# Kernel tuning notes

Hardware: AMD Instinct MI355X
Metric: run time of the kernel (lower is better)

The kernel has to match this reference:

```python
import jax, jax.numpy as jnp
import numpy as np

N = 100000
E = 1600000
D = 64  # in = hidden = out channels


def setup_inputs() -> dict:
    key = jax.random.key(0)
    ks = jax.random.split(key, 6)
    x = jax.random.normal(ks[0], (N, D), dtype=jnp.float32)
    edge_index = jax.random.randint(ks[1], (2, E), 0, N, dtype=jnp.int64)
    # bias-free linear weights, torch Linear layout [out, in]
    s = 1.0 / np.sqrt(D)
    W0 = jax.random.uniform(ks[2], (D, D), jnp.float32, -s, s)
    W1 = jax.random.uniform(ks[3], (D, D), jnp.float32, -s, s)
    Wm = jax.random.uniform(ks[4], (D, D), jnp.float32, -s, s)
    eps0 = jnp.zeros((), jnp.float32)  # train_eps=True, init 0.0
    eps1 = jnp.zeros((), jnp.float32)
    return {"x": x, "edge_index": edge_index, "W0": W0, "eps0": eps0,
            "W1": W1, "eps1": eps1, "Wm": Wm}


def reference(x, edge_index, W0, eps0, W1, eps1, Wm):
    n = x.shape[0]
    src, dst = edge_index[0], edge_index[1]

    def gin_conv(h, W, eps):
        # sparse adjacency sum-aggregation: out[i] = sum_{j->i} h[j]
        agg = jax.ops.segment_sum(h[src], dst, num_segments=n)
        # eps-scaled self-loop + bias-free linear
        return (agg + (1.0 + eps) * h) @ W.T

    h1 = jax.nn.relu(gin_conv(x, W0, eps0))   # xs[0], [N, D]
    h2 = jax.nn.relu(gin_conv(h1, W1, eps1))  # xs[1], [N, D]
    return (h1 @ Wm.T + h2) / 2.0
```

## Files before the change

### kernel.cpp

```cpp
#include <hip/hip_runtime.h>
#include <hip/hip_fp16.h>


__global__ __launch_bounds__(256) void zero_int_kernel(int* __restrict__ p, int n)
{
    int i = blockIdx.x * blockDim.x + threadIdx.x;
    int stride = gridDim.x * blockDim.x;
    for (; i < n; i += stride) p[i] = 0;
}

__global__ __launch_bounds__(256) void hist_rank_kernel(
    const int* __restrict__ dst, int* __restrict__ deg,
    int* __restrict__ rank, int E)
{
    int base = (blockIdx.x * blockDim.x + threadIdx.x) * 16;
    if (base + 15 < E) {
        int4 a = *(const int4*)&dst[base];
        int4 b = *(const int4*)&dst[base + 4];
        int4 c = *(const int4*)&dst[base + 8];
        int4 d = *(const int4*)&dst[base + 12];
        int r0 = atomicAdd(&deg[a.x], 1);
        int r1 = atomicAdd(&deg[a.y], 1);
        int r2 = atomicAdd(&deg[a.z], 1);
        int r3 = atomicAdd(&deg[a.w], 1);
        int r4 = atomicAdd(&deg[b.x], 1);
        int r5 = atomicAdd(&deg[b.y], 1);
        int r6 = atomicAdd(&deg[b.z], 1);
        int r7 = atomicAdd(&deg[b.w], 1);
        int r8 = atomicAdd(&deg[c.x], 1);
        int r9 = atomicAdd(&deg[c.y], 1);
        int rA = atomicAdd(&deg[c.z], 1);
        int rB = atomicAdd(&deg[c.w], 1);
        int rC = atomicAdd(&deg[d.x], 1);
        int rD = atomicAdd(&deg[d.y], 1);
        int rE = atomicAdd(&deg[d.z], 1);
        int rF = atomicAdd(&deg[d.w], 1);
        *(int4*)&rank[base]      = make_int4(r0, r1, r2, r3);
        *(int4*)&rank[base + 4]  = make_int4(r4, r5, r6, r7);
        *(int4*)&rank[base + 8]  = make_int4(r8, r9, rA, rB);
        *(int4*)&rank[base + 12] = make_int4(rC, rD, rE, rF);
    } else {
        for (int e = base; e < E; ++e) rank[e] = atomicAdd(&deg[dst[e]], 1);
    }
}

__global__ __launch_bounds__(256) void hist_kernel(
    const int* __restrict__ dst, int* __restrict__ deg, int E)
{
    int e4 = (blockIdx.x * blockDim.x + threadIdx.x) * 4;
    if (e4 + 3 < E) {
        int4 d = *(const int4*)&dst[e4];
        atomicAdd(&deg[d.x], 1);
        atomicAdd(&deg[d.y], 1);
        atomicAdd(&deg[d.z], 1);
        atomicAdd(&deg[d.w], 1);
    } else {
        for (int e = e4; e < E; ++e) atomicAdd(&deg[dst[e]], 1);
    }
}

__global__ __launch_bounds__(256) void scanA_kernel(
    const int* __restrict__ deg, int* __restrict__ off,
    int* __restrict__ bsum, int n)
{
    __shared__ int tmp[256];
    int t = threadIdx.x;
    int base = blockIdx.x * 1024 + t * 4;
    int v0 = 0, v1 = 0, v2 = 0, v3 = 0;
    if (base + 3 < n) {
        int4 q = *(const int4*)&deg[base];
        v0 = q.x; v1 = q.y; v2 = q.z; v3 = q.w;
    } else {
        if (base + 0 < n) v0 = deg[base + 0];
        if (base + 1 < n) v1 = deg[base + 1];
        if (base + 2 < n) v2 = deg[base + 2];
    }
    int tot = v0 + v1 + v2 + v3;
    tmp[t] = tot;
    __syncthreads();
    for (int d = 1; d < 256; d <<= 1) {
        int x = (t >= d) ? tmp[t - d] : 0;
        __syncthreads();
        tmp[t] += x;
        __syncthreads();
    }
    int incl = tmp[t];
    int p = incl - tot;
    if (base + 0 < n) off[base + 0] = p;
    if (base + 1 < n) off[base + 1] = p + v0;
    if (base + 2 < n) off[base + 2] = p + v0 + v1;
    if (base + 3 < n) off[base + 3] = p + v0 + v1 + v2;
    if (t == 255) bsum[blockIdx.x] = incl;
}

__global__ __launch_bounds__(256) void scanB_kernel(int* __restrict__ bsum, int nb)
{
    __shared__ int tmp[256];
    int t = threadIdx.x;
    int v = (t < nb) ? bsum[t] : 0;
    tmp[t] = v;
    __syncthreads();
    for (int d = 1; d < 256; d <<= 1) {
        int x = (t >= d) ? tmp[t - d] : 0;
        __syncthreads();
        tmp[t] += x;
        __syncthreads();
    }
    if (t < nb) bsum[t] = tmp[t] - v;
}

__global__ __launch_bounds__(256) void scanC_kernel(
    int* __restrict__ off, int* __restrict__ cursor,
    const int* __restrict__ bsum, int n, int E)
{
    int t = threadIdx.x;
    int add = bsum[blockIdx.x];
    int base = blockIdx.x * 1024 + t * 4;
#pragma unroll
    for (int q = 0; q < 4; ++q) {
        int idx = base + q;
        if (idx < n) {
            int v = off[idx] + add;
            off[idx] = v;
            if (cursor) cursor[idx] = v;
        }
    }
    if (blockIdx.x == 0 && t == 0) off[n] = E;
}

__global__ __launch_bounds__(256) void fill_rank_kernel(
    const int* __restrict__ src, const int* __restrict__ dst,
    const int* __restrict__ rank, const int* __restrict__ off,
    int* __restrict__ bucket, int E)
{
    int base = (blockIdx.x * blockDim.x + threadIdx.x) * 8;
    if (base + 7 < E) {
        int4 d0 = *(const int4*)&dst[base];
        int4 d1 = *(const int4*)&dst[base + 4];
        int4 r0 = *(const int4*)&rank[base];
        int4 r1 = *(const int4*)&rank[base + 4];
        int4 s0 = *(const int4*)&src[base];
        int4 s1 = *(const int4*)&src[base + 4];
        bucket[off[d0.x] + r0.x] = s0.x;
        bucket[off[d0.y] + r0.y] = s0.y;
        bucket[off[d0.z] + r0.z] = s0.z;
        bucket[off[d0.w] + r0.w] = s0.w;
        bucket[off[d1.x] + r1.x] = s1.x;
        bucket[off[d1.y] + r1.y] = s1.y;
        bucket[off[d1.z] + r1.z] = s1.z;
        bucket[off[d1.w] + r1.w] = s1.w;
    } else {
        for (int e = base; e < E; ++e) bucket[off[dst[e]] + rank[e]] = src[e];
    }
}

__global__ __launch_bounds__(256) void fill_kernel(
    const int* __restrict__ src, const int* __restrict__ dst,
    int* __restrict__ cursor, int* __restrict__ bucket, int E)
{
    int e = blockIdx.x * blockDim.x + threadIdx.x;
    if (e < E) {
        int d = dst[e];
        int p = atomicAdd(&cursor[d], 1);
        bucket[p] = src[e];
    }
}

__global__ __launch_bounds__(256) void f32_to_f16_kernel(
    const float* __restrict__ in, __half* __restrict__ out, int total4)
{
    int i = blockIdx.x * blockDim.x + threadIdx.x;
    int stride = gridDim.x * blockDim.x;
    const float4* in4 = (const float4*)in;
    uint2* out4 = (uint2*)out;
    for (; i < total4; i += stride) {
        float4 v = in4[i];
        __half2 a = __floats2half2_rn(v.x, v.y);
        __half2 b = __floats2half2_rn(v.z, v.w);
        uint2 u;
        u.x = __builtin_bit_cast(unsigned int, a);
        u.y = __builtin_bit_cast(unsigned int, b);
        out4[i] = u;
    }
}

#define WPB 8

__device__ __forceinline__ float dot4(float4 a, float4 b)
{
    return a.x * b.x + a.y * b.y + a.z * b.z + a.w * b.w;
}

__device__ __forceinline__ __half2 bc_h2(unsigned int u)
{
    return __builtin_bit_cast(__half2, u);
}

__global__ __launch_bounds__(512) void fused_gin_h_kernel(
    const __half* __restrict__ hh, const int* __restrict__ off,
    const int* __restrict__ bucket, const float* __restrict__ W,
    const float* __restrict__ eps, __half* __restrict__ outh, int n)
{
    __shared__ float Ws[64][68];
    __shared__ float P[WPB][4][64];
    __shared__ float rowbuf[WPB][64];
    int tid = threadIdx.x;
    for (int idx = tid; idx < 4096; idx += 512) Ws[idx >> 6][idx & 63] = W[idx];
    __syncthreads();
    float s = 1.0f + eps[0];
    int lane = tid & 63;
    int w = tid >> 6;
    int l16 = lane & 15;
    int g = lane >> 4;
    int wavesTotal = gridDim.x * WPB;
    for (int i = blockIdx.x * WPB + w; i < n; i += wavesTotal) {
        int2 be = *(const int2*)&off[i];
        int beg = __builtin_amdgcn_readfirstlane(be.x);
        int end = __builtin_amdgcn_readfirstlane(be.y);
        __half2 ha = bc_h2(0u), hb = bc_h2(0u);
        float4 acc4 = make_float4(0.f, 0.f, 0.f, 0.f);
        int j = beg;
        for (; j + 8 <= end; j += 8) {
            int sa = bucket[j + g];
            int sb = bucket[j + 4 + g];
            uint2 va = *(const uint2*)&hh[(size_t)sa * 64 + l16 * 4];
            uint2 vb = *(const uint2*)&hh[(size_t)sb * 64 + l16 * 4];
            ha = __hadd2(__hadd2(ha, bc_h2(va.x)), bc_h2(vb.x));
            hb = __hadd2(__hadd2(hb, bc_h2(va.y)), bc_h2(vb.y));
        }
        if (j + 4 <= end) {
            int sa = bucket[j + g];
            uint2 va = *(const uint2*)&hh[(size_t)sa * 64 + l16 * 4];
            ha = __hadd2(ha, bc_h2(va.x));
            hb = __hadd2(hb, bc_h2(va.y));
            j += 4;
        }
        if (j < end) {
            int jj = j + g;
            int sc = bucket[(jj < end) ? jj : (end - 1)];
            float m = (jj < end) ? 1.0f : 0.0f;
            uint2 vc = *(const uint2*)&hh[(size_t)sc * 64 + l16 * 4];
            float2 c01 = __half22float2(bc_h2(vc.x));
            float2 c23 = __half22float2(bc_h2(vc.y));
            acc4.x = fmaf(c01.x, m, acc4.x);
            acc4.y = fmaf(c01.y, m, acc4.y);
            acc4.z = fmaf(c23.x, m, acc4.z);
            acc4.w = fmaf(c23.y, m, acc4.w);
        }
        float2 f01 = __half22float2(ha);
        float2 f23 = __half22float2(hb);
        acc4.x += f01.x; acc4.y += f01.y; acc4.z += f23.x; acc4.w += f23.y;
        if (g == 0) {
            uint2 sv = *(const uint2*)&hh[(size_t)i * 64 + l16 * 4];
            float2 s01 = __half22float2(bc_h2(sv.x));
            float2 s23 = __half22float2(bc_h2(sv.y));
            acc4.x = fmaf(s01.x, s, acc4.x);
            acc4.y = fmaf(s01.y, s, acc4.y);
            acc4.z = fmaf(s23.x, s, acc4.z);
            acc4.w = fmaf(s23.y, s, acc4.w);
        }
        *(float4*)&P[w][g][l16 * 4] = acc4;
        __builtin_amdgcn_wave_barrier();
        float r0 = P[w][0][lane], r1 = P[w][1][lane];
        float r2 = P[w][2][lane], r3 = P[w][3][lane];
        rowbuf[w][lane] = (r0 + r1) + (r2 + r3);
        __builtin_amdgcn_wave_barrier();
        const float4* wrow = (const float4*)&Ws[lane][0];
        const float4* rrow = (const float4*)&rowbuf[w][0];
        float o = 0.f;
#pragma unroll
        for (int k4 = 0; k4 < 16; ++k4) o += dot4(wrow[k4], rrow[k4]);
        outh[(size_t)i * 64 + lane] = __float2half(fmaxf(o, 0.f));
        __builtin_amdgcn_wave_barrier();
    }
}

__global__ __launch_bounds__(512) void fused_final_h_kernel(
    const __half* __restrict__ hh1, const int* __restrict__ off,
    const int* __restrict__ bucket, const float* __restrict__ W1,
    const float* __restrict__ Wm, const float* __restrict__ eps,
    float* __restrict__ out, int n)
{
    __shared__ float W1s[64][68];
    __shared__ float Wms[64][68];
    __shared__ float P[WPB][4][64];
    __shared__ float rowbuf[WPB][64];
    __shared__ float selfbuf[WPB][64];
    int tid = threadIdx.x;
    for (int idx = tid; idx < 4096; idx += 512) {
        W1s[idx >> 6][idx & 63] = W1[idx];
        Wms[idx >> 6][idx & 63] = Wm[idx];
    }
    __syncthreads();
    float s = 1.0f + eps[0];
    int lane = tid & 63;
    int w = tid >> 6;
    int l16 = lane & 15;
    int g = lane >> 4;
    int wavesTotal = gridDim.x * WPB;
    for (int i = blockIdx.x * WPB + w; i < n; i += wavesTotal) {
        int2 be = *(const int2*)&off[i];
        int beg = __builtin_amdgcn_readfirstlane(be.x);
        int end = __builtin_amdgcn_readfirstlane(be.y);
        __half2 ha = bc_h2(0u), hb = bc_h2(0u);
        float4 acc4 = make_float4(0.f, 0.f, 0.f, 0.f);
        int j = beg;
        for (; j + 8 <= end; j += 8) {
            int sa = bucket[j + g];
            int sb = bucket[j + 4 + g];
            uint2 va = *(const uint2*)&hh1[(size_t)sa * 64 + l16 * 4];
            uint2 vb = *(const uint2*)&hh1[(size_t)sb * 64 + l16 * 4];
            ha = __hadd2(__hadd2(ha, bc_h2(va.x)), bc_h2(vb.x));
            hb = __hadd2(__hadd2(hb, bc_h2(va.y)), bc_h2(vb.y));
        }
        if (j + 4 <= end) {
            int sa = bucket[j + g];
            uint2 va = *(const uint2*)&hh1[(size_t)sa * 64 + l16 * 4];
            ha = __hadd2(ha, bc_h2(va.x));
            hb = __hadd2(hb, bc_h2(va.y));
            j += 4;
        }
        if (j < end) {
            int jj = j + g;
            int sc = bucket[(jj < end) ? jj : (end - 1)];
            float m = (jj < end) ? 1.0f : 0.0f;
            uint2 vc = *(const uint2*)&hh1[(size_t)sc * 64 + l16 * 4];
            float2 c01 = __half22float2(bc_h2(vc.x));
            float2 c23 = __half22float2(bc_h2(vc.y));
            acc4.x = fmaf(c01.x, m, acc4.x);
            acc4.y = fmaf(c01.y, m, acc4.y);
            acc4.z = fmaf(c23.x, m, acc4.z);
            acc4.w = fmaf(c23.y, m, acc4.w);
        }
        float2 f01 = __half22float2(ha);
        float2 f23 = __half22float2(hb);
        acc4.x += f01.x; acc4.y += f01.y; acc4.z += f23.x; acc4.w += f23.y;
        if (g == 0) {
            uint2 sv = *(const uint2*)&hh1[(size_t)i * 64 + l16 * 4];
            float2 s01 = __half22float2(bc_h2(sv.x));
            float2 s23 = __half22float2(bc_h2(sv.y));
            float4 sf = make_float4(s01.x, s01.y, s23.x, s23.y);
            *(float4*)&selfbuf[w][l16 * 4] = sf;
            acc4.x = fmaf(sf.x, s, acc4.x);
            acc4.y = fmaf(sf.y, s, acc4.y);
            acc4.z = fmaf(sf.z, s, acc4.z);
            acc4.w = fmaf(sf.w, s, acc4.w);
        }
        *(float4*)&P[w][g][l16 * 4] = acc4;
        __builtin_amdgcn_wave_barrier();
        float r0 = P[w][0][lane], r1 = P[w][1][lane];
        float r2 = P[w][2][lane], r3 = P[w][3][lane];
        rowbuf[w][lane] = (r0 + r1) + (r2 + r3);
        __builtin_amdgcn_wave_barrier();
        const float4* w1row = (const float4*)&W1s[lane][0];
        const float4* wmrow = (const float4*)&Wms[lane][0];
        const float4* rrow  = (const float4*)&rowbuf[w][0];
        const float4* srow  = (const float4*)&selfbuf[w][0];
        float o1 = 0.f, o2 = 0.f;
#pragma unroll
        for (int k4 = 0; k4 < 16; ++k4) {
            o1 += dot4(w1row[k4], rrow[k4]);
            o2 += dot4(wmrow[k4], srow[k4]);
        }
        out[(size_t)i * 64 + lane] = (fmaxf(o1, 0.f) + o2) * 0.5f;
        __builtin_amdgcn_wave_barrier();
    }
}

__device__ __forceinline__ float4 gather_row_f32(
    const float* __restrict__ h, const int* __restrict__ bucket,
    int beg, int end, int g, int l16, float4 acc4)
{
    int j = beg;
    for (; j + 8 <= end; j += 8) {
        int sa = bucket[j + g];
        int sb = bucket[j + 4 + g];
        float4 va = *(const float4*)&h[(size_t)sa * 64 + l16 * 4];
        float4 vb = *(const float4*)&h[(size_t)sb * 64 + l16 * 4];
        acc4.x += va.x + vb.x;
        acc4.y += va.y + vb.y;
        acc4.z += va.z + vb.z;
        acc4.w += va.w + vb.w;
    }
    if (j + 4 <= end) {
        int sa = bucket[j + g];
        float4 va = *(const float4*)&h[(size_t)sa * 64 + l16 * 4];
        acc4.x += va.x; acc4.y += va.y; acc4.z += va.z; acc4.w += va.w;
        j += 4;
    }
    if (j < end) {
        int jj = j + g;
        int sc = bucket[(jj < end) ? jj : (end - 1)];
        float m = (jj < end) ? 1.0f : 0.0f;
        float4 vc = *(const float4*)&h[(size_t)sc * 64 + l16 * 4];
        acc4.x = fmaf(vc.x, m, acc4.x);
        acc4.y = fmaf(vc.y, m, acc4.y);
        acc4.z = fmaf(vc.z, m, acc4.z);
        acc4.w = fmaf(vc.w, m, acc4.w);
    }
    return acc4;
}

__global__ __launch_bounds__(512) void fused_gin_kernel(
    const float* __restrict__ h, const int* __restrict__ off,
    const int* __restrict__ bucket, const float* __restrict__ W,
    const float* __restrict__ eps, float* __restrict__ out, int n)
{
    __shared__ float Ws[64][68];
    __shared__ float P[WPB][4][64];
    __shared__ float rowbuf[WPB][64];
    int tid = threadIdx.x;
    for (int idx = tid; idx < 4096; idx += 512) Ws[idx >> 6][idx & 63] = W[idx];
    __syncthreads();
    float s = 1.0f + eps[0];
    int lane = tid & 63;
    int w = tid >> 6;
    int l16 = lane & 15;
    int g = lane >> 4;
    int wavesTotal = gridDim.x * WPB;
    for (int i = blockIdx.x * WPB + w; i < n; i += wavesTotal) {
        float4 init = make_float4(0.f, 0.f, 0.f, 0.f);
        if (g == 0) {
            float4 self4 = *(const float4*)&h[(size_t)i * 64 + l16 * 4];
            init = make_float4(s * self4.x, s * self4.y, s * self4.z, s * self4.w);
        }
        int2 be = *(const int2*)&off[i];
        int beg = __builtin_amdgcn_readfirstlane(be.x);
        int end = __builtin_amdgcn_readfirstlane(be.y);
        float4 acc4 = gather_row_f32(h, bucket, beg, end, g, l16, init);
        *(float4*)&P[w][g][l16 * 4] = acc4;
        __builtin_amdgcn_wave_barrier();
        float r0 = P[w][0][lane], r1 = P[w][1][lane];
        float r2 = P[w][2][lane], r3 = P[w][3][lane];
        rowbuf[w][lane] = (r0 + r1) + (r2 + r3);
        __builtin_amdgcn_wave_barrier();
        const float4* wrow = (const float4*)&Ws[lane][0];
        const float4* rrow = (const float4*)&rowbuf[w][0];
        float o = 0.f;
#pragma unroll
        for (int k4 = 0; k4 < 16; ++k4) o += dot4(wrow[k4], rrow[k4]);
        out[(size_t)i * 64 + lane] = fmaxf(o, 0.f);
        __builtin_amdgcn_wave_barrier();
    }
}

__global__ __launch_bounds__(512) void fused_final_csr_kernel(
    const float* __restrict__ h1, const int* __restrict__ off,
    const int* __restrict__ bucket, const float* __restrict__ W1,
    const float* __restrict__ Wm, const float* __restrict__ eps,
    float* __restrict__ out, int n)
{
    __shared__ float W1s[64][68];
    __shared__ float Wms[64][68];
    __shared__ float P[WPB][4][64];
    __shared__ float rowbuf[WPB][64];
    __shared__ float selfbuf[WPB][64];
    int tid = threadIdx.x;
    for (int idx = tid; idx < 4096; idx += 512) {
        W1s[idx >> 6][idx & 63] = W1[idx];
        Wms[idx >> 6][idx & 63] = Wm[idx];
    }
    __syncthreads();
    float s = 1.0f + eps[0];
    int lane = tid & 63;
    int w = tid >> 6;
    int l16 = lane & 15;
    int g = lane >> 4;
    int wavesTotal = gridDim.x * WPB;
    for (int i = blockIdx.x * WPB + w; i < n; i += wavesTotal) {
        float4 init = make_float4(0.f, 0.f, 0.f, 0.f);
        if (g == 0) {
            float4 self4 = *(const float4*)&h1[(size_t)i * 64 + l16 * 4];
            *(float4*)&selfbuf[w][l16 * 4] = self4;
            init = make_float4(s * self4.x, s * self4.y, s * self4.z, s * self4.w);
        }
        int2 be = *(const int2*)&off[i];
        int beg = __builtin_amdgcn_readfirstlane(be.x);
        int end = __builtin_amdgcn_readfirstlane(be.y);
        float4 acc4 = gather_row_f32(h1, bucket, beg, end, g, l16, init);
        *(float4*)&P[w][g][l16 * 4] = acc4;
        __builtin_amdgcn_wave_barrier();
        float r0 = P[w][0][lane], r1 = P[w][1][lane];
        float r2 = P[w][2][lane], r3 = P[w][3][lane];
        rowbuf[w][lane] = (r0 + r1) + (r2 + r3);
        __builtin_amdgcn_wave_barrier();
        const float4* w1row = (const float4*)&W1s[lane][0];
        const float4* wmrow = (const float4*)&Wms[lane][0];
        const float4* rrow  = (const float4*)&rowbuf[w][0];
        const float4* srow  = (const float4*)&selfbuf[w][0];
        float o1 = 0.f, o2 = 0.f;
#pragma unroll
        for (int k4 = 0; k4 < 16; ++k4) {
            o1 += dot4(w1row[k4], rrow[k4]);
            o2 += dot4(wmrow[k4], srow[k4]);
        }
        out[(size_t)i * 64 + lane] = (fmaxf(o1, 0.f) + o2) * 0.5f;
        __builtin_amdgcn_wave_barrier();
    }
}

__global__ __launch_bounds__(256) void init_scale_kernel(
    const float* __restrict__ h, const float* __restrict__ eps,
    float* __restrict__ agg, int total4)
{
    float s = 1.0f + eps[0];
    int i = blockIdx.x * blockDim.x + threadIdx.x;
    int stride = gridDim.x * blockDim.x;
    const float4* h4 = (const float4*)h;
    float4* a4 = (float4*)agg;
    for (; i < total4; i += stride) {
        float4 v = h4[i];
        v.x *= s; v.y *= s; v.z *= s; v.w *= s;
        a4[i] = v;
    }
}

__global__ __launch_bounds__(256) void scatter_kernel(
    const float* __restrict__ h, const int* __restrict__ src,
    const int* __restrict__ dst, float* __restrict__ agg, int E)
{
    int lane = threadIdx.x & 63;
    int e = blockIdx.x * 4 + (threadIdx.x >> 6);
    if (e >= E) return;
    int s = src[e];
    int d = dst[e];
    atomicAdd(&agg[(size_t)d * 64 + lane], h[(size_t)s * 64 + lane]);
}

__global__ __launch_bounds__(256) void gemm_relu_kernel(
    const float* __restrict__ A, const float* __restrict__ W,
    float* __restrict__ out, int n)
{
    __shared__ float Wt[64][65];
    __shared__ float rowbuf[4][64];
    int tid = threadIdx.x;
    for (int i = tid; i < 4096; i += 256) Wt[i & 63][i >> 6] = W[i];
    __syncthreads();
    int lane = tid & 63;
    int w = tid >> 6;
    int wavesTotal = gridDim.x * 4;
    for (int i = blockIdx.x * 4 + w; i < n; i += wavesTotal) {
        rowbuf[w][lane] = A[(size_t)i * 64 + lane];
        __builtin_amdgcn_wave_barrier();
        float o = 0.f;
#pragma unroll
        for (int k = 0; k < 64; ++k) o += rowbuf[w][k] * Wt[k][lane];
        out[(size_t)i * 64 + lane] = fmaxf(o, 0.f);
        __builtin_amdgcn_wave_barrier();
    }
}

__global__ __launch_bounds__(256) void final_kernel(
    const float* __restrict__ Agg, const float* __restrict__ H1,
    const float* __restrict__ W1, const float* __restrict__ Wm,
    float* __restrict__ out, int n)
{
    __shared__ float W1t[64][65];
    __shared__ float Wmt[64][65];
    __shared__ float rowbuf[4][64];
    __shared__ float selfbuf[4][64];
    int tid = threadIdx.x;
    for (int i = tid; i < 4096; i += 256) {
        W1t[i & 63][i >> 6] = W1[i];
        Wmt[i & 63][i >> 6] = Wm[i];
    }
    __syncthreads();
    int lane = tid & 63;
    int w = tid >> 6;
    int wavesTotal = gridDim.x * 4;
    for (int i = blockIdx.x * 4 + w; i < n; i += wavesTotal) {
        rowbuf[w][lane] = Agg[(size_t)i * 64 + lane];
        selfbuf[w][lane] = H1[(size_t)i * 64 + lane];
        __builtin_amdgcn_wave_barrier();
        float o1 = 0.f, o2 = 0.f;
#pragma unroll
        for (int k = 0; k < 64; ++k) {
            o1 += rowbuf[w][k] * W1t[k][lane];
            o2 += selfbuf[w][k] * Wmt[k][lane];
        }
        out[(size_t)i * 64 + lane] = (fmaxf(o1, 0.f) + o2) * 0.5f;
        __builtin_amdgcn_wave_barrier();
    }
}

extern "C" void kernel_launch(void* const* d_in, const int* in_sizes, int n_in,
                              void* d_out, int out_size, void* d_ws, size_t ws_size,
                              hipStream_t stream)
{
    const float* x    = (const float*)d_in[0];
    const int*   ei   = (const int*)d_in[1];
    const float* W0   = (const float*)d_in[2];
    const float* eps0 = (const float*)d_in[3];
    const float* W1   = (const float*)d_in[4];
    const float* eps1 = (const float*)d_in[5];
    const float* Wm   = (const float*)d_in[6];
    float* out = (float*)d_out;

    int n = in_sizes[0] / 64;
    int E = in_sizes[1] / 2;
    const int* src = ei;
    const int* dst = ei + E;

    auto align1k = [](size_t v) { return (v + 1023) & ~(size_t)1023; };

    size_t hhx_off    = 0;
    size_t hh1_off    = align1k(hhx_off + (size_t)n * 64 * 2);
    size_t off_off    = align1k(hh1_off + (size_t)n * 64 * 2);
    size_t deg_off    = align1k(off_off + (size_t)(n + 1) * 4);
    size_t bsum_off   = align1k(deg_off + (size_t)n * 4);
    size_t bucket_off = align1k(bsum_off + 256 * 4);
    size_t rank_off   = align1k(bucket_off + (size_t)E * 4);
    size_t need_A2    = rank_off + (size_t)E * 4;

    size_t b_h1_off     = 0;
    size_t b_off_off    = align1k(b_h1_off + (size_t)n * 64 * 4);
    size_t b_deg_off    = align1k(b_off_off + (size_t)(n + 1) * 4);
    size_t b_cursor_off = align1k(b_deg_off + (size_t)n * 4);
    size_t b_bsum_off   = align1k(b_cursor_off + (size_t)n * 4);
    size_t b_bucket_off = align1k(b_bsum_off + 256 * 4);
    size_t need_B       = b_bucket_off + (size_t)E * 4;

    int nb = (n + 1023) / 1024;
    int e8Blocks  = (E + 2047) / 2048;
    int e16Blocks = (E + 4095) / 4096;
    int total4 = n * 16;

    if (ws_size >= need_A2) {
        __half* hhx  = (__half*)((char*)d_ws + hhx_off);
        __half* hh1  = (__half*)((char*)d_ws + hh1_off);
        int* off     = (int*)((char*)d_ws + off_off);
        int* deg     = (int*)((char*)d_ws + deg_off);
        int* bsum    = (int*)((char*)d_ws + bsum_off);
        int* bucket  = (int*)((char*)d_ws + bucket_off);
        int* rank    = (int*)((char*)d_ws + rank_off);

        zero_int_kernel<<<256, 256, 0, stream>>>(deg, n);
        f32_to_f16_kernel<<<2048, 256, 0, stream>>>(x, hhx, total4);
        hist_rank_kernel<<<e16Blocks, 256, 0, stream>>>(dst, deg, rank, E);
        scanA_kernel<<<nb, 256, 0, stream>>>(deg, off, bsum, n);
        scanB_kernel<<<1, 256, 0, stream>>>(bsum, nb);
        scanC_kernel<<<nb, 256, 0, stream>>>(off, (int*)nullptr, bsum, n, E);
        fill_rank_kernel<<<e8Blocks, 256, 0, stream>>>(src, dst, rank, off, bucket, E);

        fused_gin_h_kernel<<<1024, 512, 0, stream>>>(hhx, off, bucket, W0, eps0, hh1, n);
        fused_final_h_kernel<<<768, 512, 0, stream>>>(hh1, off, bucket, W1, Wm, eps1, out, n);
    } else if (ws_size >= need_B) {
        float* h1    = (float*)((char*)d_ws + b_h1_off);
        int* off     = (int*)((char*)d_ws + b_off_off);
        int* deg     = (int*)((char*)d_ws + b_deg_off);
        int* cursor  = (int*)((char*)d_ws + b_cursor_off);
        int* bsum    = (int*)((char*)d_ws + b_bsum_off);
        int* bucket  = (int*)((char*)d_ws + b_bucket_off);

        zero_int_kernel<<<256, 256, 0, stream>>>(deg, n);
        hist_kernel<<<(E + 1023) / 1024, 256, 0, stream>>>(dst, deg, E);
        scanA_kernel<<<nb, 256, 0, stream>>>(deg, off, bsum, n);
        scanB_kernel<<<1, 256, 0, stream>>>(bsum, nb);
        scanC_kernel<<<nb, 256, 0, stream>>>(off, cursor, bsum, n, E);
        fill_kernel<<<(E + 255) / 256, 256, 0, stream>>>(src, dst, cursor, bucket, E);

        fused_gin_kernel<<<1024, 512, 0, stream>>>(x, off, bucket, W0, eps0, h1, n);
        fused_final_csr_kernel<<<768, 512, 0, stream>>>(h1, off, bucket, W1, Wm, eps1, out, n);
    } else {
        float* agg = (float*)d_ws;
        float* h1  = out;
        int scatterBlocks = (E + 3) / 4;

        init_scale_kernel<<<2048, 256, 0, stream>>>(x, eps0, agg, total4);
        scatter_kernel<<<scatterBlocks, 256, 0, stream>>>(x, src, dst, agg, E);
        gemm_relu_kernel<<<2048, 256, 0, stream>>>(agg, W0, h1, n);
        init_scale_kernel<<<2048, 256, 0, stream>>>(h1, eps1, agg, total4);
        scatter_kernel<<<scatterBlocks, 256, 0, stream>>>(h1, src, dst, agg, E);
        final_kernel<<<2048, 256, 0, stream>>>(agg, h1, W1, Wm, out, n);
    }
}
```

Measured before the change: 241.8 us.

## Gather with 16-byte half loads, shuffle-reduce, and fp16 dot2 for the linear layer

Each lane now loads 8 halves (uint4) per neighbor row, so eight neighbors are in flight per wave instead of four. Partial sums are combined with xor-shuffles in fp16 instead of going through an fp32 LDS buffer. Weights are stored in LDS as fp16 in a column-blocked layout and the 64x64 matvec uses fdot2 instructions. This halves LDS traffic and ALU work per output. The trade-off is that the self-loop term and the neighbor reduction are now done entirely in fp16, which adds rounding error. The final kernel's grid is also raised to 1024 blocks.

Measured after the change: 225.2 us. 1.07x faster.

```diff
diff --git a/kernel.cpp b/kernel.cpp
--- a/kernel.cpp
+++ b/kernel.cpp
@@ -186,90 +186,130 @@
 
 #define WPB 8
 
-__device__ __forceinline__ float dot4(float4 a, float4 b)
-{
-    return a.x * b.x + a.y * b.y + a.z * b.z + a.w * b.w;
-}
-
 __device__ __forceinline__ __half2 bc_h2(unsigned int u)
 {
     return __builtin_bit_cast(__half2, u);
 }
+__device__ __forceinline__ unsigned int bc_u(__half2 h)
+{
+    return __builtin_bit_cast(unsigned int, h);
+}
+
+#if __has_builtin(__builtin_amdgcn_fdot2)
+typedef _Float16 half2_v __attribute__((ext_vector_type(2)));
+__device__ __forceinline__ float fdot2(unsigned int a, unsigned int b, float c)
+{
+    return __builtin_amdgcn_fdot2(__builtin_bit_cast(half2_v, a),
+                                  __builtin_bit_cast(half2_v, b), c, false);
+}
+#else
+__device__ __forceinline__ float fdot2(unsigned int a, unsigned int b, float c)
+{
+    float2 af = __half22float2(bc_h2(a));
+    float2 bf = __half22float2(bc_h2(b));
+    return fmaf(af.x, bf.x, fmaf(af.y, bf.y, c));
+}
+#endif
+
+__device__ __forceinline__ void xreduce4(__half2& a0, __half2& a1,
+                                         __half2& a2, __half2& a3)
+{
+#pragma unroll
+    for (int mask = 8; mask <= 32; mask <<= 1) {
+        a0 = __hadd2(a0, bc_h2((unsigned int)__shfl_xor((int)bc_u(a0), mask, 64)));
+        a1 = __hadd2(a1, bc_h2((unsigned int)__shfl_xor((int)bc_u(a1), mask, 64)));
+        a2 = __hadd2(a2, bc_h2((unsigned int)__shfl_xor((int)bc_u(a2), mask, 64)));
+        a3 = __hadd2(a3, bc_h2((unsigned int)__shfl_xor((int)bc_u(a3), mask, 64)));
+    }
+}
+
+__device__ __forceinline__ void gather8(
+    const __half* __restrict__ hh, const int* __restrict__ bucket,
+    int beg, int end, int g, int l8,
+    __half2& a0, __half2& a1, __half2& a2, __half2& a3)
+{
+    int j = beg;
+    for (; j + 16 <= end; j += 16) {
+        int sa = bucket[j + g];
+        int sb = bucket[j + 8 + g];
+        uint4 va = *(const uint4*)&hh[(size_t)sa * 64 + l8 * 8];
+        uint4 vb = *(const uint4*)&hh[(size_t)sb * 64 + l8 * 8];
+        a0 = __hadd2(__hadd2(a0, bc_h2(va.x)), bc_h2(vb.x));
+        a1 = __hadd2(__hadd2(a1, bc_h2(va.y)), bc_h2(vb.y));
+        a2 = __hadd2(__hadd2(a2, bc_h2(va.z)), bc_h2(vb.z));
+        a3 = __hadd2(__hadd2(a3, bc_h2(va.w)), bc_h2(vb.w));
+    }
+    if (j + 8 <= end) {
+        int sa = bucket[j + g];
+        uint4 va = *(const uint4*)&hh[(size_t)sa * 64 + l8 * 8];
+        a0 = __hadd2(a0, bc_h2(va.x));
+        a1 = __hadd2(a1, bc_h2(va.y));
+        a2 = __hadd2(a2, bc_h2(va.z));
+        a3 = __hadd2(a3, bc_h2(va.w));
+        j += 8;
+    }
+    if (j < end) {
+        int jj = j + g;
+        int sc = bucket[(jj < end) ? jj : (end - 1)];
+        __half2 m2 = __float2half2_rn((jj < end) ? 1.0f : 0.0f);
+        uint4 vc = *(const uint4*)&hh[(size_t)sc * 64 + l8 * 8];
+        a0 = __hfma2(bc_h2(vc.x), m2, a0);
+        a1 = __hfma2(bc_h2(vc.y), m2, a1);
+        a2 = __hfma2(bc_h2(vc.z), m2, a2);
+        a3 = __hfma2(bc_h2(vc.w), m2, a3);
+    }
+}
+
 
 __global__ __launch_bounds__(512) void fused_gin_h_kernel(
     const __half* __restrict__ hh, const int* __restrict__ off,
     const int* __restrict__ bucket, const float* __restrict__ W,
     const float* __restrict__ eps, __half* __restrict__ outh, int n)
 {
-    __shared__ float Ws[64][68];
-    __shared__ float P[WPB][4][64];
-    __shared__ float rowbuf[WPB][64];
+    __shared__ __half WhS[4096];
+    __shared__ __half rowh[WPB][64];
     int tid = threadIdx.x;
-    for (int idx = tid; idx < 4096; idx += 512) Ws[idx >> 6][idx & 63] = W[idx];
+    for (int idx = tid; idx < 4096; idx += 512) {
+        int row = idx >> 6, col = idx & 63;
+        WhS[(col >> 3) * 512 + row * 8 + (col & 7)] = __float2half(W[idx]);
+    }
     __syncthreads();
     float s = 1.0f + eps[0];
+    __half2 s2 = __float2half2_rn(s);
     int lane = tid & 63;
     int w = tid >> 6;
-    int l16 = lane & 15;
-    int g = lane >> 4;
+    int l8 = lane & 7;
+    int g = lane >> 3;
     int wavesTotal = gridDim.x * WPB;
+    const uint4* Wh4 = (const uint4*)WhS;
     for (int i = blockIdx.x * WPB + w; i < n; i += wavesTotal) {
         int2 be = *(const int2*)&off[i];
         int beg = __builtin_amdgcn_readfirstlane(be.x);
         int end = __builtin_amdgcn_readfirstlane(be.y);
-        __half2 ha = bc_h2(0u), hb = bc_h2(0u);
-        float4 acc4 = make_float4(0.f, 0.f, 0.f, 0.f);
-        int j = beg;
-        for (; j + 8 <= end; j += 8) {
-            int sa = bucket[j + g];
-            int sb = bucket[j + 4 + g];
-            uint2 va = *(const uint2*)&hh[(size_t)sa * 64 + l16 * 4];
-            uint2 vb = *(const uint2*)&hh[(size_t)sb * 64 + l16 * 4];
-            ha = __hadd2(__hadd2(ha, bc_h2(va.x)), bc_h2(vb.x));
-            hb = __hadd2(__hadd2(hb, bc_h2(va.y)), bc_h2(vb.y));
-        }
-        if (j + 4 <= end) {
-            int sa = bucket[j + g];
-            uint2 va = *(const uint2*)&hh[(size_t)sa * 64 + l16 * 4];
-            ha = __hadd2(ha, bc_h2(va.x));
-            hb = __hadd2(hb, bc_h2(va.y));
-            j += 4;
-        }
-        if (j < end) {
-            int jj = j + g;
-            int sc = bucket[(jj < end) ? jj : (end - 1)];
-            float m = (jj < end) ? 1.0f : 0.0f;
-            uint2 vc = *(const uint2*)&hh[(size_t)sc * 64 + l16 * 4];
-            float2 c01 = __half22float2(bc_h2(vc.x));
-            float2 c23 = __half22float2(bc_h2(vc.y));
-            acc4.x = fmaf(c01.x, m, acc4.x);
-            acc4.y = fmaf(c01.y, m, acc4.y);
-            acc4.z = fmaf(c23.x, m, acc4.z);
-            acc4.w = fmaf(c23.y, m, acc4.w);
-        }
-        float2 f01 = __half22float2(ha);
-        float2 f23 = __half22float2(hb);
-        acc4.x += f01.x; acc4.y += f01.y; acc4.z += f23.x; acc4.w += f23.y;
+        __half2 a0 = bc_h2(0u), a1 = bc_h2(0u), a2 = bc_h2(0u), a3 = bc_h2(0u);
+        gather8(hh, bucket, beg, end, g, l8, a0, a1, a2, a3);
+        xreduce4(a0, a1, a2, a3);
         if (g == 0) {
-            uint2 sv = *(const uint2*)&hh[(size_t)i * 64 + l16 * 4];
-            float2 s01 = __half22float2(bc_h2(sv.x));
-            float2 s23 = __half22float2(bc_h2(sv.y));
-            acc4.x = fmaf(s01.x, s, acc4.x);
-            acc4.y = fmaf(s01.y, s, acc4.y);
-            acc4.z = fmaf(s23.x, s, acc4.z);
-            acc4.w = fmaf(s23.y, s, acc4.w);
-        }
-        *(float4*)&P[w][g][l16 * 4] = acc4;
-        __builtin_amdgcn_wave_barrier();
-        float r0 = P[w][0][lane], r1 = P[w][1][lane];
-        float r2 = P[w][2][lane], r3 = P[w][3][lane];
-        rowbuf[w][lane] = (r0 + r1) + (r2 + r3);
-        __builtin_amdgcn_wave_barrier();
-        const float4* wrow = (const float4*)&Ws[lane][0];
-        const float4* rrow = (const float4*)&rowbuf[w][0];
+            uint4 sv = *(const uint4*)&hh[(size_t)i * 64 + l8 * 8];
+            a0 = __hfma2(bc_h2(sv.x), s2, a0);
+            a1 = __hfma2(bc_h2(sv.y), s2, a1);
+            a2 = __hfma2(bc_h2(sv.z), s2, a2);
+            a3 = __hfma2(bc_h2(sv.w), s2, a3);
+            uint4 st;
+            st.x = bc_u(a0); st.y = bc_u(a1); st.z = bc_u(a2); st.w = bc_u(a3);
+            *(uint4*)&rowh[w][l8 * 8] = st;
+        }
+        __builtin_amdgcn_wave_barrier();
         float o = 0.f;
 #pragma unroll
-        for (int k4 = 0; k4 < 16; ++k4) o += dot4(wrow[k4], rrow[k4]);
+        for (int k4 = 0; k4 < 8; ++k4) {
+            uint4 wv = Wh4[k4 * 64 + lane];
+            uint4 rv = *(const uint4*)&rowh[w][k4 * 8];
+            o = fdot2(wv.x, rv.x, o);
+            o = fdot2(wv.y, rv.y, o);
+            o = fdot2(wv.z, rv.z, o);
+            o = fdot2(wv.w, rv.w, o);
+        }
         outh[(size_t)i * 64 + lane] = __float2half(fmaxf(o, 0.f));
         __builtin_amdgcn_wave_barrier();
     }
@@ -281,90 +321,70 @@
     const float* __restrict__ Wm, const float* __restrict__ eps,
     float* __restrict__ out, int n)
 {
-    __shared__ float W1s[64][68];
-    __shared__ float Wms[64][68];
-    __shared__ float P[WPB][4][64];
-    __shared__ float rowbuf[WPB][64];
-    __shared__ float selfbuf[WPB][64];
+    __shared__ __half W1hS[4096];
+    __shared__ __half WmhS[4096];
+    __shared__ __half rowh[WPB][64];
+    __shared__ __half selfh[WPB][64];
     int tid = threadIdx.x;
     for (int idx = tid; idx < 4096; idx += 512) {
-        W1s[idx >> 6][idx & 63] = W1[idx];
-        Wms[idx >> 6][idx & 63] = Wm[idx];
+        int row = idx >> 6, col = idx & 63;
+        int li = (col >> 3) * 512 + row * 8 + (col & 7);
+        W1hS[li] = __float2half(W1[idx]);
+        WmhS[li] = __float2half(Wm[idx]);
     }
     __syncthreads();
     float s = 1.0f + eps[0];
+    __half2 s2 = __float2half2_rn(s);
     int lane = tid & 63;
     int w = tid >> 6;
-    int l16 = lane & 15;
-    int g = lane >> 4;
+    int l8 = lane & 7;
+    int g = lane >> 3;
     int wavesTotal = gridDim.x * WPB;
+    const uint4* W1h4 = (const uint4*)W1hS;
+    const uint4* Wmh4 = (const uint4*)WmhS;
     for (int i = blockIdx.x * WPB + w; i < n; i += wavesTotal) {
         int2 be = *(const int2*)&off[i];
         int beg = __builtin_amdgcn_readfirstlane(be.x);
         int end = __builtin_amdgcn_readfirstlane(be.y);
-        __half2 ha = bc_h2(0u), hb = bc_h2(0u);
-        float4 acc4 = make_float4(0.f, 0.f, 0.f, 0.f);
-        int j = beg;
-        for (; j + 8 <= end; j += 8) {
-            int sa = bucket[j + g];
-            int sb = bucket[j + 4 + g];
-            uint2 va = *(const uint2*)&hh1[(size_t)sa * 64 + l16 * 4];
-            uint2 vb = *(const uint2*)&hh1[(size_t)sb * 64 + l16 * 4];
-            ha = __hadd2(__hadd2(ha, bc_h2(va.x)), bc_h2(vb.x));
-            hb = __hadd2(__hadd2(hb, bc_h2(va.y)), bc_h2(vb.y));
-        }
-        if (j + 4 <= end) {
-            int sa = bucket[j + g];
-            uint2 va = *(const uint2*)&hh1[(size_t)sa * 64 + l16 * 4];
-            ha = __hadd2(ha, bc_h2(va.x));
-            hb = __hadd2(hb, bc_h2(va.y));
-            j += 4;
-        }
-        if (j < end) {
-            int jj = j + g;
-            int sc = bucket[(jj < end) ? jj : (end - 1)];
-            float m = (jj < end) ? 1.0f : 0.0f;
-            uint2 vc = *(const uint2*)&hh1[(size_t)sc * 64 + l16 * 4];
-            float2 c01 = __half22float2(bc_h2(vc.x));
-            float2 c23 = __half22float2(bc_h2(vc.y));
-            acc4.x = fmaf(c01.x, m, acc4.x);
-            acc4.y = fmaf(c01.y, m, acc4.y);
-            acc4.z = fmaf(c23.x, m, acc4.z);
-            acc4.w = fmaf(c23.y, m, acc4.w);
-        }
-        float2 f01 = __half22float2(ha);
-        float2 f23 = __half22float2(hb);
-        acc4.x += f01.x; acc4.y += f01.y; acc4.z += f23.x; acc4.w += f23.y;
+        __half2 a0 = bc_h2(0u), a1 = bc_h2(0u), a2 = bc_h2(0u), a3 = bc_h2(0u);
+        gather8(hh1, bucket, beg, end, g, l8, a0, a1, a2, a3);
+        xreduce4(a0, a1, a2, a3);
         if (g == 0) {
-            uint2 sv = *(const uint2*)&hh1[(size_t)i * 64 + l16 * 4];
-            float2 s01 = __half22float2(bc_h2(sv.x));
-            float2 s23 = __half22float2(bc_h2(sv.y));
-            float4 sf = make_float4(s01.x, s01.y, s23.x, s23.y);
-            *(float4*)&selfbuf[w][l16 * 4] = sf;
-            acc4.x = fmaf(sf.x, s, acc4.x);
-            acc4.y = fmaf(sf.y, s, acc4.y);
-            acc4.z = fmaf(sf.z, s, acc4.z);
-            acc4.w = fmaf(sf.w, s, acc4.w);
-        }
-        *(float4*)&P[w][g][l16 * 4] = acc4;
-        __builtin_amdgcn_wave_barrier();
-        float r0 = P[w][0][lane], r1 = P[w][1][lane];
-        float r2 = P[w][2][lane], r3 = P[w][3][lane];
-        rowbuf[w][lane] = (r0 + r1) + (r2 + r3);
-        __builtin_amdgcn_wave_barrier();
-        const float4* w1row = (const float4*)&W1s[lane][0];
-        const float4* wmrow = (const float4*)&Wms[lane][0];
-        const float4* rrow  = (const float4*)&rowbuf[w][0];
-        const float4* srow  = (const float4*)&selfbuf[w][0];
+            uint4 sv = *(const uint4*)&hh1[(size_t)i * 64 + l8 * 8];
+            *(uint4*)&selfh[w][l8 * 8] = sv;
+            a0 = __hfma2(bc_h2(sv.x), s2, a0);
+            a1 = __hfma2(bc_h2(sv.y), s2, a1);
+            a2 = __hfma2(bc_h2(sv.z), s2, a2);
+            a3 = __hfma2(bc_h2(sv.w), s2, a3);
+            uint4 st;
+            st.x = bc_u(a0); st.y = bc_u(a1); st.z = bc_u(a2); st.w = bc_u(a3);
+            *(uint4*)&rowh[w][l8 * 8] = st;
+        }
+        __builtin_amdgcn_wave_barrier();
         float o1 = 0.f, o2 = 0.f;
 #pragma unroll
-        for (int k4 = 0; k4 < 16; ++k4) {
-            o1 += dot4(w1row[k4], rrow[k4]);
-            o2 += dot4(wmrow[k4], srow[k4]);
+        for (int k4 = 0; k4 < 8; ++k4) {
+            uint4 wv1 = W1h4[k4 * 64 + lane];
+            uint4 wv2 = Wmh4[k4 * 64 + lane];
+            uint4 rv  = *(const uint4*)&rowh[w][k4 * 8];
+            uint4 sv  = *(const uint4*)&selfh[w][k4 * 8];
+            o1 = fdot2(wv1.x, rv.x, o1);
+            o1 = fdot2(wv1.y, rv.y, o1);
+            o1 = fdot2(wv1.z, rv.z, o1);
+            o1 = fdot2(wv1.w, rv.w, o1);
+            o2 = fdot2(wv2.x, sv.x, o2);
+            o2 = fdot2(wv2.y, sv.y, o2);
+            o2 = fdot2(wv2.z, sv.z, o2);
+            o2 = fdot2(wv2.w, sv.w, o2);
         }
         out[(size_t)i * 64 + lane] = (fmaxf(o1, 0.f) + o2) * 0.5f;
         __builtin_amdgcn_wave_barrier();
     }
+}
+
+__device__ __forceinline__ float dot4(float4 a, float4 b)
+{
+    return a.x * b.x + a.y * b.y + a.z * b.z + a.w * b.w;
 }
 
 __device__ __forceinline__ float4 gather_row_f32(
@@ -643,7 +663,7 @@
         fill_rank_kernel<<<e8Blocks, 256, 0, stream>>>(src, dst, rank, off, bucket, E);
 
         fused_gin_h_kernel<<<1024, 512, 0, stream>>>(hhx, off, bucket, W0, eps0, hh1, n);
-        fused_final_h_kernel<<<768, 512, 0, stream>>>(hh1, off, bucket, W1, Wm, eps1, out, n);
+        fused_final_h_kernel<<<1024, 512, 0, stream>>>(hh1, off, bucket, W1, Wm, eps1, out, n);
     } else if (ws_size >= need_B) {
         float* h1    = (float*)((char*)d_ws + b_h1_off);
         int* off     = (int*)((char*)d_ws + b_off_off);
```
